# Kernel tuning notes

Hardware: AMD Instinct MI355X
Metric: run time of the kernel (lower is better)

Reference implementation:

```python
import jax, jax.numpy as jnp
import numpy as np

ALPHA = 0.2  # LeakyReLU negative slope
NEG = -9e15

def _gat_head(Wh, a1, a2, adj_mask):
    # Wh: [N,O], a1/a2: [O], adj_mask: [N,N] bool
    e = jax.nn.leaky_relu(jnp.einsum('no,o->n', Wh, a1)[:, None]
                          + jnp.einsum('no,o->n', Wh, a2)[None, :], ALPHA)
    att = jax.nn.softmax(jnp.where(adj_mask, e, NEG), axis=-1)
    return att @ Wh  # [N,O]

def setup_inputs() -> dict:
    key = jax.random.key(0)
    ks = jax.random.split(key, 6)
    N, F_IN, O, H, C = 4096, 512, 64, 8, 16
    x = jax.random.normal(ks[0], (N, F_IN), jnp.float32)
    adj = jax.random.randint(ks[1], (N, N), 0, 2, jnp.int32)
    W = jax.random.normal(ks[2], (H, F_IN, O), jnp.float32) * 0.05
    a = jax.random.normal(ks[3], (H, 2 * O), jnp.float32) * 0.05
    W_out = jax.random.normal(ks[4], (H * O, C), jnp.float32) * 0.05
    a_out = jax.random.normal(ks[5], (2 * C,), jnp.float32) * 0.05
    return {'x': x, 'adj': adj, 'W': W, 'a': a, 'W_out': W_out, 'a_out': a_out}

def reference(x, adj, W, a, W_out, a_out):
    N = x.shape[0]
    H, _, O = W.shape
    C = W_out.shape[1]
    mask = adj > 0  # [N,N]
    # multi-head attention layer (vmapped over heads)
    Wh = jnp.einsum('nf,hfo->hno', x, W)  # [H,N,O]
    a1, a2 = a[:, :O], a[:, O:]
    h_heads = jax.vmap(_gat_head, in_axes=(0, 0, 0, None))(Wh, a1, a2, mask)  # [H,N,O]
    h = jax.nn.elu(h_heads)  # concat=True -> elu per head
    h = jnp.transpose(h, (1, 0, 2)).reshape(N, H * O)  # concat heads
    # output attention layer (concat=False)
    Wh_o = h @ W_out  # [N,C]
    out = _gat_head(Wh_o, a_out[:C], a_out[C:], mask)  # [N,C]
    out = jax.nn.elu(out)
    return jax.nn.log_softmax(out, axis=1)
```

## Files before the change

### kernel.cpp

```cpp
#include <hip/hip_runtime.h>
#include <string.h>


typedef _Float16 h2 __attribute__((ext_vector_type(2)));
typedef _Float16 half8 __attribute__((ext_vector_type(8)));
typedef __attribute__((ext_vector_type(4))) float f32x4;
typedef unsigned long long u64;
typedef unsigned short u16;
typedef unsigned int u32;

__device__ __forceinline__ u16 f2h(float f){
  union { _Float16 h; u16 u; } c; c.h = (_Float16)f; return c.u;
}
__device__ __forceinline__ h2 u2h2(u32 u){ union { u32 u; h2 h; } c; c.u = u; return c.h; }
__device__ __forceinline__ u32 h22u(h2 h){ union { u32 u; h2 h; } c; c.h = h; return c.u; }
__device__ __forceinline__ half8 pk2h8(uint4 v){ union { uint4 u; half8 h; } c; c.u = v; return c.h; }

__device__ __forceinline__ void async16(void* lds, const void* g){
  __builtin_amdgcn_global_load_lds((const __attribute__((address_space(1))) u32*)g,
                                   (__attribute__((address_space(3))) u32*)lds, 16, 0, 0);
}
__device__ __forceinline__ void async4(void* lds, const void* g){
  __builtin_amdgcn_global_load_lds((const __attribute__((address_space(1))) u32*)g,
                                   (__attribute__((address_space(3))) u32*)lds, 4, 0, 0);
}

__global__ __launch_bounds__(256) void k_gemm1(const float* __restrict__ x,
                                               const float* __restrict__ W,
                                               const float* __restrict__ av,
                                               const int* __restrict__ adj,
                                               u16* __restrict__ whB,
                                               u64* __restrict__ bits_t,
                                               float* __restrict__ r1,
                                               u16* __restrict__ e21h, u16* __restrict__ e202h){
  __shared__ u16 wLDS[32768];
  __shared__ u16 tr[4096];
  int h    = blockIdx.y;
  int nblk = blockIdx.x;
  int tid  = threadIdx.x;
  int lane = tid & 63;
  int wv   = tid >> 6;
  int row16 = lane & 15, grp = lane >> 4;
  int n0 = nblk * 64;
  int n0w = n0 + wv * 16;

  {
    int o = tid & 63, fb0 = tid >> 6;
    for (int k = 0; k < 16; ++k){
      int fgb = fb0 + k * 4;
      const float* src = W + ((size_t)h * 512 + fgb * 8) * 64 + o;
      u32 pk[4];
      #pragma unroll
      for (int p = 0; p < 4; ++p)
        pk[p] = (u32)f2h(src[(2 * p) * 64]) | ((u32)f2h(src[(2 * p + 1) * 64]) << 16);
      *(uint4*)(wLDS + ((size_t)fgb * 64 + o) * 8) = *(uint4*)pk;
    }
  }
  __syncthreads();

  f32x4 acc[4] = {};
  #pragma unroll 4
  for (int ks = 0; ks < 16; ++ks){
    int fgb = ks * 4 + grp;
    const float* xs = x + (size_t)(n0w + row16) * 512 + fgb * 8;
    float4 xv0 = ((const float4*)xs)[0];
    float4 xv1 = ((const float4*)xs)[1];
    u32 ax[4];
    ax[0] = (u32)f2h(xv0.x) | ((u32)f2h(xv0.y) << 16);
    ax[1] = (u32)f2h(xv0.z) | ((u32)f2h(xv0.w) << 16);
    ax[2] = (u32)f2h(xv1.x) | ((u32)f2h(xv1.y) << 16);
    ax[3] = (u32)f2h(xv1.z) | ((u32)f2h(xv1.w) << 16);
    half8 af = pk2h8(*(uint4*)ax);
    #pragma unroll
    for (int nt = 0; nt < 4; ++nt){
      half8 bf = *(const half8*)(wLDS + ((size_t)fgb * 64 + nt * 16 + row16) * 8);
      acc[nt] = __builtin_amdgcn_mfma_f32_16x16x32_f16(af, bf, acc[nt], 0, 0, 0);
    }
  }
  float a1v[4], a2v[4];
  #pragma unroll
  for (int nt = 0; nt < 4; ++nt){
    a1v[nt] = av[h * 128 + nt * 16 + row16];
    a2v[nt] = av[h * 128 + 64 + nt * 16 + row16];
  }
  #pragma unroll
  for (int r = 0; r < 4; ++r){
    float p1 = acc[0][r]*a1v[0] + acc[1][r]*a1v[1] + acc[2][r]*a1v[2] + acc[3][r]*a1v[3];
    float p2 = acc[0][r]*a2v[0] + acc[1][r]*a2v[1] + acc[2][r]*a2v[2] + acc[3][r]*a2v[3];
    #pragma unroll
    for (int d = 1; d < 16; d <<= 1){ p1 += __shfl_xor(p1, d, 64); p2 += __shfl_xor(p2, d, 64); }
    if (row16 == 0){
      int idx = h * 4096 + n0w + grp * 4 + r;
      r1[idx]    = __expf(-0.8f * p1);
      e21h[idx]  = f2h(__expf(p2));
      e202h[idx] = f2h(__expf(0.2f * p2));
    }
  }
  #pragma unroll
  for (int nt = 0; nt < 4; ++nt)
    #pragma unroll
    for (int r = 0; r < 4; ++r){
      int jl = wv * 16 + grp * 4 + r;
      int o  = nt * 16 + row16;
      tr[((jl >> 3) * 64 + o) * 8 + (jl & 7)] = f2h(acc[nt][r]);
    }
  __syncthreads();
  u16* dst = whB + (size_t)h * 262144 + (size_t)n0 * 64;
  #pragma unroll
  for (int q = 0; q < 2; ++q)
    *(uint4*)(dst + (tid * 2 + q) * 8) = *(const uint4*)(tr + (tid * 2 + q) * 8);

  {
    int B = blockIdx.y * 64 + blockIdx.x;
    int uid0 = B * 512 + wv * 128;
    for (int k = 0; k < 128; k += 8){
      int v[8];
      #pragma unroll
      for (int q = 0; q < 8; ++q){
        int uid = uid0 + k + q;
        v[q] = adj[(size_t)(uid >> 6) * 4096 + ((uid & 63) << 6) + lane];
      }
      u64 m[8];
      #pragma unroll
      for (int q = 0; q < 8; ++q) m[q] = __ballot(v[q] != 0);
      if (lane == 0){
        #pragma unroll
        for (int q = 0; q < 8; ++q){
          int uid = uid0 + k + q;
          bits_t[(size_t)(uid & 63) * 4096 + (uid >> 6)] = m[q];
        }
      }
    }
  }
}

__global__ __launch_bounds__(256) void k_att1(const u16* __restrict__ whB,
                                              const u64* __restrict__ bits_t,
                                              const float* __restrict__ r1,
                                              const u16* __restrict__ e21h, const u16* __restrict__ e202h,
                                              u16* __restrict__ pnum, float* __restrict__ pden){
  __shared__ u16  smB[2][4096];
  __shared__ u32  smT[2][2][64];
  __shared__ u32  smLut[4];
  int h     = blockIdx.y;
  int iblk  = blockIdx.x;
  int split = blockIdx.z;
  int lane = threadIdx.x & 63;
  int wv   = threadIdx.x >> 6;
  int row16 = lane & 15, grp = lane >> 4;
  if (threadIdx.x < 4)
    smLut[threadIdx.x] = ((threadIdx.x & 1) ? 0xFFFFu : 0u) | ((threadIdx.x & 2) ? 0xFFFF0000u : 0u);
  int i = iblk * 64 + wv * 16 + row16;
  int hoff = h * 4096;
  u32 rb = (u32)f2h(r1[hoff + i]); rb |= rb << 16;
  h2 rr = u2h2(rb);
  const u16* whBh = whB + (size_t)h * 262144;
  int jbeg = split * 1024;

  half8 bden;
  {
    u32 z[4] = {0,0,0,0};
    if (row16 == 0){ z[0]=0x3C003C00u; z[1]=0x3C003C00u; z[2]=0x3C003C00u; z[3]=0x3C003C00u; }
    bden = pk2h8(*(uint4*)z);
  }

  auto stage = [&](int bb, int j0){
    const char* g = (const char*)whBh + (size_t)j0 * 128 + wv * 2048 + lane * 16;
    char* l = (char*)(&smB[bb][0]) + wv * 2048;
    async16(l, g);
    async16(l + 1024, g + 1024);
    if (wv == 0)      async4(&smT[bb][0][0], (const char*)(e21h  + hoff + j0) + lane * 4);
    else if (wv == 1) async4(&smT[bb][1][0], (const char*)(e202h + hoff + j0) + lane * 4);
  };

  f32x4 acc[4] = {};
  f32x4 accden = {};
  stage(0, jbeg);
  for (int c = 0; c < 16; ++c){
    int bb = c & 1;
    u64 mrow = bits_t[(size_t)(split * 16 + c) * 4096 + i];
    __syncthreads();
    if (c < 15) stage(bb ^ 1, jbeg + (c + 1) * 64);
    #pragma unroll
    for (int ks = 0; ks < 2; ++ks){
      uint4 e1q = *(const uint4*)((const char*)&smT[bb][0][0] + ks * 64 + grp * 16);
      uint4 e2q = *(const uint4*)((const char*)&smT[bb][1][0] + ks * 64 + grp * 16);
      u32 es[4] = {e1q.x, e1q.y, e1q.z, e1q.w};
      u32 gs[4] = {e2q.x, e2q.y, e2q.z, e2q.w};
      const u16* bbase = &smB[bb][(ks * 4 + grp) * 512];
      half8 bf0 = *(const half8*)(bbase + (0 * 16 + row16) * 8);
      half8 bf1 = *(const half8*)(bbase + (1 * 16 + row16) * 8);
      half8 bf2 = *(const half8*)(bbase + (2 * 16 + row16) * 8);
      half8 bf3 = *(const half8*)(bbase + (3 * 16 + row16) * 8);
      u32 mb = ((u32)(mrow >> (ks * 32)) >> (grp * 8)) & 0xffu;
      u32 pk[4];
      #pragma unroll
      for (int t2i = 0; t2i < 4; ++t2i){
        h2 w = __builtin_elementwise_max(u2h2(es[t2i]), rr * u2h2(gs[t2i]));
        pk[t2i] = h22u(w) & smLut[(mb >> (2 * t2i)) & 3u];
      }
      half8 af = pk2h8(*(uint4*)pk);
      acc[0] = __builtin_amdgcn_mfma_f32_16x16x32_f16(af, bf0, acc[0], 0, 0, 0);
      acc[1] = __builtin_amdgcn_mfma_f32_16x16x32_f16(af, bf1, acc[1], 0, 0, 0);
      acc[2] = __builtin_amdgcn_mfma_f32_16x16x32_f16(af, bf2, acc[2], 0, 0, 0);
      acc[3] = __builtin_amdgcn_mfma_f32_16x16x32_f16(af, bf3, acc[3], 0, 0, 0);
      accden = __builtin_amdgcn_mfma_f32_16x16x32_f16(af, bden, accden, 0, 0, 0);
    }
  }

  #pragma unroll
  for (int r4 = 0; r4 < 4; ++r4){
    int n = iblk * 64 + wv * 16 + grp * 4 + r4;
    if (row16 == 0)
      pden[((size_t)split * 8 + h) * 4096 + n] = accden[r4];
    u16* dst = pnum + ((size_t)split * 4096 + n) * 512 + h * 64 + row16;
    #pragma unroll
    for (int nt = 0; nt < 4; ++nt)
      dst[nt * 16] = f2h(acc[nt][r4]);
  }
}

__global__ __launch_bounds__(256) void k_gemm2(const u16* __restrict__ pnum,
                                               const float* __restrict__ pden,
                                               const float* __restrict__ Wout,
                                               const float* __restrict__ aout,
                                               u16* __restrict__ whoB,
                                               float* __restrict__ r1o,
                                               u16* __restrict__ e21oh, u16* __restrict__ e202oh){
  __shared__ float Wl[8192];
  __shared__ float hrow[16 * 516];
  __shared__ float sden[128];
  int n0 = blockIdx.x * 16;
  for (int t = threadIdx.x; t < 8192; t += 256) Wl[t] = Wout[t];
  if (threadIdx.x < 128){
    int hh = threadIdx.x >> 4, nn = threadIdx.x & 15;
    float d = 0.f;
    #pragma unroll
    for (int s = 0; s < 4; ++s) d += pden[((size_t)s * 8 + hh) * 4096 + n0 + nn];
    sden[threadIdx.x] = d;
  }
  __syncthreads();
  {
    int nn = threadIdx.x >> 4;
    int fc = threadIdx.x & 15;
    int f0 = fc * 32;
    int hh = fc >> 1;
    float dinv = 1.f / sden[hh * 16 + nn];
    float v[32];
    #pragma unroll
    for (int k = 0; k < 32; ++k) v[k] = 0.f;
    #pragma unroll
    for (int s = 0; s < 4; ++s){
      const u16* p = pnum + ((size_t)s * 4096 + n0 + nn) * 512 + f0;
      #pragma unroll
      for (int q = 0; q < 4; ++q){
        uint4 raw = *(const uint4*)(p + q * 8);
        u32 rw[4] = {raw.x, raw.y, raw.z, raw.w};
        #pragma unroll
        for (int d2 = 0; d2 < 4; ++d2){
          h2 dh = u2h2(rw[d2]);
          v[q * 8 + d2 * 2]     += (float)dh.x;
          v[q * 8 + d2 * 2 + 1] += (float)dh.y;
        }
      }
    }
    #pragma unroll
    for (int k = 0; k < 32; ++k){
      float val = v[k] * dinv;
      val = val > 0.f ? val : (__expf(val) - 1.f);
      hrow[nn * 516 + f0 + k] = val;
    }
  }
  __syncthreads();
  int c  = threadIdx.x & 15;
  int rl = threadIdx.x >> 4;
  int n = n0 + rl;
  const float4* hr = (const float4*)(hrow + rl * 516);
  float acc = 0.f;
  #pragma unroll 8
  for (int f4 = 0; f4 < 128; ++f4){
    float4 hv = hr[f4];
    int f = f4 * 4;
    acc += hv.x * Wl[f * 16 + c] + hv.y * Wl[(f + 1) * 16 + c]
         + hv.z * Wl[(f + 2) * 16 + c] + hv.w * Wl[(f + 3) * 16 + c];
  }
  whoB[((size_t)(n >> 3) * 16 + c) * 8 + (n & 7)] = f2h(acc);
  float p1 = acc * aout[c], p2 = acc * aout[16 + c];
  #pragma unroll
  for (int d = 1; d < 16; d <<= 1){ p1 += __shfl_xor(p1, d, 64); p2 += __shfl_xor(p2, d, 64); }
  if (c == 0){
    r1o[n]    = __expf(-0.8f * p1);
    e21oh[n]  = f2h(__expf(p2));
    e202oh[n] = f2h(__expf(0.2f * p2));
  }
}

__global__ __launch_bounds__(256) void k_att2(const u16* __restrict__ whoB,
                                              const u64* __restrict__ bits_t,
                                              const float* __restrict__ r1o,
                                              const u16* __restrict__ e21oh, const u16* __restrict__ e202oh,
                                              float* __restrict__ pnum, float* __restrict__ pden){
  __shared__ u32 smLut[4];
  int iblk  = blockIdx.x;
  int split = blockIdx.y;
  int lane = threadIdx.x & 63;
  int wv   = threadIdx.x >> 6;
  int row16 = lane & 15, grp = lane >> 4;
  if (threadIdx.x < 4)
    smLut[threadIdx.x] = ((threadIdx.x & 1) ? 0xFFFFu : 0u) | ((threadIdx.x & 2) ? 0xFFFF0000u : 0u);
  __syncthreads();
  int i = iblk * 64 + wv * 16 + row16;
  u32 rb = (u32)f2h(r1o[i]); rb |= rb << 16;
  h2 rr = u2h2(rb);
  int jbeg = split * 256;
  half8 bden;
  {
    u32 z[4] = {0,0,0,0};
    if (row16 == 0){ z[0]=0x3C003C00u; z[1]=0x3C003C00u; z[2]=0x3C003C00u; z[3]=0x3C003C00u; }
    bden = pk2h8(*(uint4*)z);
  }

  f32x4 acc = {};
  f32x4 accden = {};
  #pragma unroll
  for (int c = 0; c < 4; ++c){
    int j0 = jbeg + c * 64;
    u64 mrow = bits_t[(size_t)(split * 4 + c) * 4096 + i];
    #pragma unroll
    for (int ks = 0; ks < 2; ++ks){
      int sb = (j0 >> 3) + ks * 4 + grp;
      half8 bf = *(const half8*)(whoB + ((size_t)sb * 16 + row16) * 8);
      uint4 e1q = *(const uint4*)(e21oh  + j0 + ks * 32 + grp * 8);
      uint4 e2q = *(const uint4*)(e202oh + j0 + ks * 32 + grp * 8);
      u32 es[4] = {e1q.x, e1q.y, e1q.z, e1q.w};
      u32 gs[4] = {e2q.x, e2q.y, e2q.z, e2q.w};
      u32 mb = ((u32)(mrow >> (ks * 32)) >> (grp * 8)) & 0xffu;
      u32 pk[4];
      #pragma unroll
      for (int t2i = 0; t2i < 4; ++t2i){
        h2 w = __builtin_elementwise_max(u2h2(es[t2i]), rr * u2h2(gs[t2i]));
        pk[t2i] = h22u(w) & smLut[(mb >> (2 * t2i)) & 3u];
      }
      half8 af = pk2h8(*(uint4*)pk);
      acc    = __builtin_amdgcn_mfma_f32_16x16x32_f16(af, bf, acc, 0, 0, 0);
      accden = __builtin_amdgcn_mfma_f32_16x16x32_f16(af, bden, accden, 0, 0, 0);
    }
  }
  #pragma unroll
  for (int r4 = 0; r4 < 4; ++r4){
    int n = iblk * 64 + wv * 16 + grp * 4 + r4;
    if (row16 == 0)
      pden[(size_t)n * 16 + split] = accden[r4];
    pnum[((size_t)n * 16 + split) * 16 + row16] = acc[r4];
  }
}

__global__ __launch_bounds__(256) void k_final(const float* __restrict__ pnum,
                                               const float* __restrict__ pden,
                                               float* __restrict__ out){
  int tid = blockIdx.x * 256 + threadIdx.x;
  int c = tid & 15;
  int n = tid >> 4;
  float num = 0.f, den = 0.f;
  #pragma unroll
  for (int s = 0; s < 16; ++s){
    num += pnum[((size_t)n * 16 + s) * 16 + c];
    den += pden[(size_t)n * 16 + s];
  }
  float v = num / den;
  v = v > 0.f ? v : (__expf(v) - 1.f);
  float m = v;
  #pragma unroll
  for (int d = 1; d < 16; d <<= 1) m = fmaxf(m, __shfl_xor(m, d, 64));
  float es = __expf(v - m), ss = es;
  #pragma unroll
  for (int d = 1; d < 16; d <<= 1) ss += __shfl_xor(ss, d, 64);
  out[(size_t)n * 16 + c] = v - m - __logf(ss);
}

extern "C" void kernel_launch(void* const* d_in, const int* in_sizes, int n_in,
                              void* d_out, int out_size, void* d_ws, size_t ws_size,
                              hipStream_t stream){
  (void)in_sizes; (void)n_in; (void)out_size; (void)ws_size;
  const float* x    = (const float*)d_in[0];
  const int*   adj  = (const int*)d_in[1];
  const float* W    = (const float*)d_in[2];
  const float* av   = (const float*)d_in[3];
  const float* Wout = (const float*)d_in[4];
  const float* aout = (const float*)d_in[5];
  float* out = (float*)d_out;
  char* ws = (char*)d_ws;

  u64*  bits_t  = (u64*)(ws + 0x0000000);
  u16*  whB     = (u16*)(ws + 0x0200000);
  float* r1     = (float*)(ws + 0x0600000);
  u16*  e21h    = (u16*)(ws + 0x0620000);
  u16*  e202h   = (u16*)(ws + 0x0630000);
  u16*  pnum1   = (u16*)(ws + 0x0680000);
  float* pden1  = (float*)(ws + 0x1680000);
  u16*  whoB    = (u16*)(ws + 0x1700000);
  float* r1o    = (float*)(ws + 0x1720000);
  u16*  e21oh   = (u16*)(ws + 0x1724000);
  u16*  e202oh  = (u16*)(ws + 0x1726000);
  float* pnum2  = (float*)(ws + 0x1730000);
  float* pden2  = (float*)(ws + 0x1B30000);

  k_gemm1<<<dim3(64, 8), dim3(256), 0, stream>>>(x, W, av, adj, whB, bits_t, r1, e21h, e202h);
  k_att1<<<dim3(64, 8, 4), dim3(256), 0, stream>>>(whB, bits_t, r1, e21h, e202h, pnum1, pden1);
  k_gemm2<<<dim3(256), dim3(256), 0, stream>>>(pnum1, pden1, Wout, aout, whoB, r1o, e21oh, e202oh);
  k_att2<<<dim3(64, 16), dim3(256), 0, stream>>>(whoB, bits_t, r1o, e21oh, e202oh, pnum2, pden2);
  k_final<<<dim3(256), dim3(256), 0, stream>>>(pnum2, pden2, out);
}
```

Measured before the change: 175.4 us.

## Fuse output attention layer with final normalization via in-block split-K reduction

Replaces the 16-way split output-attention kernel and the separate final kernel with one kernel. Each block handles 16 rows, with its four waves each covering a quarter of the columns, and reduces the partial numerators and denominators through shared memory before applying ELU and log-softmax. This removes a kernel launch and the global round trip of the partial sums. In exchange the grid shrinks from 1024 to 256 blocks and each wave runs a longer serial loop, which may reduce latency hiding.

```diff
diff --git a/kernel.cpp b/kernel.cpp
--- a/kernel.cpp
+++ b/kernel.cpp
@@ -1,5 +1,4 @@
 #include <hip/hip_runtime.h>
-#include <string.h>
 
 
 typedef _Float16 h2 __attribute__((ext_vector_type(2)));
@@ -295,24 +294,24 @@
   }
 }
 
-__global__ __launch_bounds__(256) void k_att2(const u16* __restrict__ whoB,
-                                              const u64* __restrict__ bits_t,
-                                              const float* __restrict__ r1o,
-                                              const u16* __restrict__ e21oh, const u16* __restrict__ e202oh,
-                                              float* __restrict__ pnum, float* __restrict__ pden){
+__global__ __launch_bounds__(256) void k_att2f(const u16* __restrict__ whoB,
+                                               const u64* __restrict__ bits_t,
+                                               const float* __restrict__ r1o,
+                                               const u16* __restrict__ e21oh, const u16* __restrict__ e202oh,
+                                               float* __restrict__ out){
+  __shared__ float s_acc[4][16][16];
+  __shared__ float s_den[4][16];
   __shared__ u32 smLut[4];
-  int iblk  = blockIdx.x;
-  int split = blockIdx.y;
-  int lane = threadIdx.x & 63;
-  int wv   = threadIdx.x >> 6;
+  int n0 = blockIdx.x * 16;
+  int tid = threadIdx.x;
+  int lane = tid & 63, wv = tid >> 6;
   int row16 = lane & 15, grp = lane >> 4;
-  if (threadIdx.x < 4)
-    smLut[threadIdx.x] = ((threadIdx.x & 1) ? 0xFFFFu : 0u) | ((threadIdx.x & 2) ? 0xFFFF0000u : 0u);
-  __syncthreads();
-  int i = iblk * 64 + wv * 16 + row16;
+  if (tid < 4)
+    smLut[tid] = ((tid & 1) ? 0xFFFFu : 0u) | ((tid & 2) ? 0xFFFF0000u : 0u);
+  __syncthreads();
+  int i = n0 + row16;
   u32 rb = (u32)f2h(r1o[i]); rb |= rb << 16;
   h2 rr = u2h2(rb);
-  int jbeg = split * 256;
   half8 bden;
   {
     u32 z[4] = {0,0,0,0};
@@ -322,10 +321,10 @@
 
   f32x4 acc = {};
   f32x4 accden = {};
-  #pragma unroll
-  for (int c = 0; c < 4; ++c){
-    int j0 = jbeg + c * 64;
-    u64 mrow = bits_t[(size_t)(split * 4 + c) * 4096 + i];
+  int jbase = wv * 1024;
+  for (int c = 0; c < 16; ++c){
+    int j0 = jbase + c * 64;
+    u64 mrow = bits_t[(size_t)(wv * 16 + c) * 4096 + i];
     #pragma unroll
     for (int ks = 0; ks < 2; ++ks){
       int sb = (j0 >> 3) + ks * 4 + grp;
@@ -348,34 +347,26 @@
   }
   #pragma unroll
   for (int r4 = 0; r4 < 4; ++r4){
-    int n = iblk * 64 + wv * 16 + grp * 4 + r4;
-    if (row16 == 0)
-      pden[(size_t)n * 16 + split] = accden[r4];
-    pnum[((size_t)n * 16 + split) * 16 + row16] = acc[r4];
-  }
-}
-
-__global__ __launch_bounds__(256) void k_final(const float* __restrict__ pnum,
-                                               const float* __restrict__ pden,
-                                               float* __restrict__ out){
-  int tid = blockIdx.x * 256 + threadIdx.x;
-  int c = tid & 15;
-  int n = tid >> 4;
-  float num = 0.f, den = 0.f;
-  #pragma unroll
-  for (int s = 0; s < 16; ++s){
-    num += pnum[((size_t)n * 16 + s) * 16 + c];
-    den += pden[(size_t)n * 16 + s];
-  }
-  float v = num / den;
-  v = v > 0.f ? v : (__expf(v) - 1.f);
-  float m = v;
-  #pragma unroll
-  for (int d = 1; d < 16; d <<= 1) m = fmaxf(m, __shfl_xor(m, d, 64));
-  float es = __expf(v - m), ss = es;
-  #pragma unroll
-  for (int d = 1; d < 16; d <<= 1) ss += __shfl_xor(ss, d, 64);
-  out[(size_t)n * 16 + c] = v - m - __logf(ss);
+    s_acc[wv][grp * 4 + r4][row16] = acc[r4];
+    if (row16 == 0) s_den[wv][grp * 4 + r4] = accden[r4];
+  }
+  __syncthreads();
+  {
+    int row = tid >> 4, c = tid & 15;
+    if (tid < 256){
+      float num = s_acc[0][row][c] + s_acc[1][row][c] + s_acc[2][row][c] + s_acc[3][row][c];
+      float den = s_den[0][row] + s_den[1][row] + s_den[2][row] + s_den[3][row];
+      float v = num / den;
+      v = v > 0.f ? v : (__expf(v) - 1.f);
+      float m = v;
+      #pragma unroll
+      for (int d = 1; d < 16; d <<= 1) m = fmaxf(m, __shfl_xor(m, d, 64));
+      float es = __expf(v - m), ss = es;
+      #pragma unroll
+      for (int d = 1; d < 16; d <<= 1) ss += __shfl_xor(ss, d, 64);
+      out[(size_t)(n0 + row) * 16 + c] = v - m - __logf(ss);
+    }
+  }
 }
 
 extern "C" void kernel_launch(void* const* d_in, const int* in_sizes, int n_in,
@@ -402,12 +393,9 @@
   float* r1o    = (float*)(ws + 0x1720000);
   u16*  e21oh   = (u16*)(ws + 0x1724000);
   u16*  e202oh  = (u16*)(ws + 0x1726000);
-  float* pnum2  = (float*)(ws + 0x1730000);
-  float* pden2  = (float*)(ws + 0x1B30000);
 
   k_gemm1<<<dim3(64, 8), dim3(256), 0, stream>>>(x, W, av, adj, whB, bits_t, r1, e21h, e202h);
   k_att1<<<dim3(64, 8, 4), dim3(256), 0, stream>>>(whB, bits_t, r1, e21h, e202h, pnum1, pden1);
   k_gemm2<<<dim3(256), dim3(256), 0, stream>>>(pnum1, pden1, Wout, aout, whoB, r1o, e21oh, e202oh);
-  k_att2<<<dim3(64, 16), dim3(256), 0, stream>>>(whoB, bits_t, r1o, e21oh, e202oh, pnum2, pden2);
-  k_final<<<dim3(256), dim3(256), 0, stream>>>(pnum2, pden2, out);
-}
+  k_att2f<<<dim3(256), dim3(256), 0, stream>>>(whoB, bits_t, r1o, e21oh, e202oh, out);
+}
```

New measurement: 179.3 us. 1.02x slower.
